# Kernel tuning notes

Hardware: AMD Instinct MI355X
Metric: run time of the kernel (lower is better)

The kernel has to match this reference:

```python
import jax, jax.numpy as jnp
import numpy as np

B, C, T = 16, 192, 4096
K = 5
L = 16


def conv1d(x, w, b, pad):
    # x: [B, Cin, T], w: [Cout, Cin, K] -> [B, Cout, T]
    y = jax.lax.conv_general_dilated(
        x, w, window_strides=(1,), padding=[(pad, pad)],
        dimension_numbers=("NCH", "OIH", "NCH"))
    return y + b[None, :, None]


def setup_inputs() -> dict:
    key = jax.random.key(0)
    ks = jax.random.split(key, 8)
    scale = 0.1
    x = jax.random.normal(ks[0], (B, C, T), dtype=jnp.float32)
    mask = jnp.ones((B, 1, T), dtype=jnp.float32)
    # in_layers: Conv1d(C -> 2C, K), stacked over layers (weight-norm folded)
    W_in = jax.random.normal(ks[1], (L, 2 * C, C, K), dtype=jnp.float32) * scale
    b_in = jax.random.normal(ks[2], (L, 2 * C), dtype=jnp.float32) * scale
    # res_skip layers 0..L-2: Conv1d(C -> 2C, 1)
    W_rs = jax.random.normal(ks[3], (L - 1, 2 * C, C, 1), dtype=jnp.float32) * scale
    b_rs = jax.random.normal(ks[4], (L - 1, 2 * C), dtype=jnp.float32) * scale
    # last res_skip layer: Conv1d(C -> C, 1)
    W_last = jax.random.normal(ks[5], (C, C, 1), dtype=jnp.float32) * scale
    b_last = jax.random.normal(ks[6], (C,), dtype=jnp.float32) * scale
    return {"x": x, "mask": mask, "W_in": W_in, "b_in": b_in,
            "W_rs": W_rs, "b_rs": b_rs, "W_last": W_last, "b_last": b_last}


def reference(x, mask, W_in, b_in, W_rs, b_rs, W_last, b_last):
    pad = K // 2  # dilation_rate == 1, so padding is 'same'
    o = jnp.zeros_like(x)
    for i in range(L):
        x_in = conv1d(x, W_in[i], b_in[i], pad)          # [B, 2C, T]
        x1, x2 = x_in[:, :C], x_in[:, C:]
        acts = jnp.tanh(x1) * jax.nn.sigmoid(x2)          # gated activation (dropout=0)
        if i == L - 1:
            o = o + conv1d(acts, W_last, b_last, 0)
        else:
            rs = conv1d(acts, W_rs[i], b_rs[i], 0)        # [B, 2C, T]
            x = (x + rs[:, :C]) * mask                    # residual
            o = o + rs[:, C:]                              # skip
    return o * mask
```

## Files before the change

kernel.cpp:

```cpp
#include <hip/hip_runtime.h>
#include <hip/hip_bf16.h>

#define C 192
#define T 4096
#define L 16
#define BATCH 16
#define NT 64
#define XR 72
#define CPAD 200

#define CONV_TAP_STRIDE 73728
#define MT_STRIDE       3072
#define ICC_STRIDE      512

typedef __attribute__((ext_vector_type(8))) _Float16 half8;
typedef __attribute__((ext_vector_type(4))) _Float16 half4;
typedef __attribute__((ext_vector_type(4))) float f32x4;

__device__ __forceinline__ float gatefn(float x1, float x2) {
    float ax = fabsf(x1);
    float e  = __expf(-2.f * ax);
    float th = __builtin_copysignf((1.f - e) / (1.f + e), x1);
    float sg = 1.f / (1.f + __expf(-x2));
    return th * sg;
}

__global__ __launch_bounds__(256)
void fmt_win(const float* __restrict__ W, _Float16* __restrict__ dst, int total) {
    int gid = blockIdx.x * 256 + threadIdx.x;
    if (gid >= total) return;
    int lane = gid & 63; int r = gid >> 6;
    int icc = r % 6; r /= 6;
    int mt  = r % 24; r /= 24;
    int tap = r % 5;  int l = r / 5;
    int oc  = mt * 16 + (lane & 15);
    int ic0 = icc * 32 + (lane >> 4) * 8;
    const float* s = W + ((size_t)((l * 384 + oc) * 192 + ic0)) * 5 + tap;
    half8 v;
    #pragma unroll
    for (int i = 0; i < 8; ++i) v[i] = (_Float16)s[(size_t)i * 5];
    *reinterpret_cast<half8*>(dst + (size_t)gid * 8) = v;
}

__global__ __launch_bounds__(256)
void fmt_w11(const float* __restrict__ W, _Float16* __restrict__ dst, int mtc, int total) {
    int gid = blockIdx.x * 256 + threadIdx.x;
    if (gid >= total) return;
    int lane = gid & 63; int r = gid >> 6;
    int icc = r % 6; r /= 6;
    int mt  = r % mtc; int l = r / mtc;
    int oc  = mt * 16 + (lane & 15);
    int ic0 = icc * 32 + (lane >> 4) * 8;
    const float* s = W + (size_t)(l * (mtc * 16) + oc) * 192 + ic0;
    half8 v;
    #pragma unroll
    for (int i = 0; i < 8; ++i) v[i] = (_Float16)s[i];
    *reinterpret_cast<half8*>(dst + (size_t)gid * 8) = v;
}

__global__ __launch_bounds__(256)
void xpose(const float* __restrict__ x, _Float16* __restrict__ xh, _Float16* __restrict__ xl)
{
    __shared__ float tile[C][65];
    const int t0 = blockIdx.x * 64;
    const int b  = blockIdx.y;
    const float* xg = x + (size_t)b * C * T;
    for (int idx = threadIdx.x; idx < C * 16; idx += 256) {
        int ch = idx & 15, c = idx >> 4;
        f32x4 v = *reinterpret_cast<const f32x4*>(xg + (size_t)c * T + t0 + ch * 4);
        #pragma unroll
        for (int q = 0; q < 4; ++q) tile[c][ch * 4 + q] = v[q];
    }
    __syncthreads();
    for (int idx = threadIdx.x; idx < 64 * 24; idx += 256) {
        int cc = idx % 24, t = idx / 24;
        half8 h8, l8;
        #pragma unroll
        for (int i = 0; i < 8; ++i) {
            float v = tile[cc * 8 + i][t];
            _Float16 h = (_Float16)v;
            h8[i] = h;
            l8[i] = (_Float16)(v - (float)h);
        }
        size_t off = (size_t)b * T * C + (size_t)(t0 + t) * C + cc * 8;
        *reinterpret_cast<half8*>(xh + off) = h8;
        *reinterpret_cast<half8*>(xl + off) = l8;
    }
}

template<bool FIRST, bool LAST>
__global__ __launch_bounds__(256, 2)
void wnet_layer(const _Float16* __restrict__ xhin, const _Float16* __restrict__ xlin,
                _Float16* __restrict__ xhout, _Float16* __restrict__ xlout,
                const float* __restrict__ mask,
                const _Float16* __restrict__ wc,
                const float* __restrict__ bc,
                const _Float16* __restrict__ wr,
                const float* __restrict__ br,
                float* __restrict__ o)
{
    __shared__ __align__(16) _Float16 xhi[XR * CPAD];

    const int tid = threadIdx.x;
    const int t0  = blockIdx.x * NT;
    const int b   = blockIdx.y;

    {
        const _Float16* gh = xhin + (size_t)b * T * C;
        for (int idx = tid; idx < XR * 24; idx += 256) {
            int chunk = idx % 24;
            int r     = idx / 24;
            int t = t0 - 4 + r;
            half8 v = {};
            if (t >= 0 && t < T)
                v = *reinterpret_cast<const half8*>(gh + (size_t)t * C + chunk * 8);
            *reinterpret_cast<half8*>(&xhi[r * CPAD + chunk * 8]) = v;
        }
    }
    __syncthreads();

    const int lane = tid & 63;
    const int wm   = tid >> 6;
    const int col  = lane & 15;
    const int sg   = lane >> 4;

    int wbase[6];
    #pragma unroll
    for (int q = 0; q < 6; ++q) {
        int h = q / 3, j = q % 3;
        int mt = h * 12 + wm * 3 + j;
        wbase[q] = mt * MT_STRIDE + lane * 8;
    }

    f32x4 acc[3][2][4];
    #pragma unroll
    for (int j = 0; j < 3; ++j)
    #pragma unroll
    for (int h = 0; h < 2; ++h) {
        f32x4 bv = *reinterpret_cast<const f32x4*>(bc + (h * 12 + wm * 3 + j) * 16 + sg * 4);
        #pragma unroll
        for (int p = 0; p < 4; ++p) acc[j][h][p] = bv;
    }

    half8 hA[6], hB[6];
    #pragma unroll
    for (int q = 0; q < 6; ++q)
        hA[q] = *reinterpret_cast<const half8*>(wc + wbase[q]);

    auto convstep = [&](int icc, half8 (&curH)[6], half8 (&nxtH)[6],
                        size_t tapoff, size_t ntapoff, int tap) {
        const size_t coff = tapoff + (size_t)icc * ICC_STRIDE;
        const size_t noff = (icc == 5) ? ntapoff : coff + ICC_STRIDE;
        #pragma unroll
        for (int q = 0; q < 6; ++q)
            nxtH[q] = *reinterpret_cast<const half8*>(wc + noff + wbase[q]);
        half8 bh[4];
        #pragma unroll
        for (int p = 0; p < 4; ++p) {
            int off = (p * 16 + col + tap + 2) * CPAD + icc * 32 + sg * 8;
            bh[p] = *reinterpret_cast<const half8*>(&xhi[off]);
        }
        __builtin_amdgcn_sched_barrier(0);
        __builtin_amdgcn_s_setprio(1);
        #pragma unroll
        for (int h = 0; h < 2; ++h)
        #pragma unroll
        for (int j = 0; j < 3; ++j)
        #pragma unroll
        for (int p = 0; p < 4; ++p)
            acc[j][h][p] = __builtin_amdgcn_mfma_f32_16x16x32_f16(
                curH[h * 3 + j], bh[p], acc[j][h][p], 0, 0, 0);
        __builtin_amdgcn_s_setprio(0);
    };

    for (int tap = 0; tap < 5; ++tap) {
        const size_t tapoff  = (size_t)tap * CONV_TAP_STRIDE;
        const size_t ntapoff = (size_t)(tap < 4 ? tap + 1 : 4) * CONV_TAP_STRIDE;
        #pragma unroll
        for (int ih = 0; ih < 3; ++ih) {
            convstep(2 * ih,     hA, hB, tapoff, ntapoff, tap);
            convstep(2 * ih + 1, hB, hA, tapoff, ntapoff, tap);
        }
    }

    half4 xresh[3][4];
    if constexpr (!LAST) {
        #pragma unroll
        for (int p = 0; p < 4; ++p) {
            const int row = p * 16 + col + 4;
            #pragma unroll
            for (int j = 0; j < 3; ++j) {
                const int ch = (wm * 3 + j) * 16 + sg * 4;
                xresh[j][p] = *reinterpret_cast<const half4*>(&xhi[row * CPAD + ch]);
            }
        }
    }
    __syncthreads();

    #pragma unroll
    for (int j = 0; j < 3; ++j)
    #pragma unroll
    for (int p = 0; p < 4; ++p) {
        const int tt = p * 16 + col;
        const int ch = (wm * 3 + j) * 16 + sg * 4;
        half4 av;
        #pragma unroll
        for (int i = 0; i < 4; ++i)
            av[i] = (_Float16)gatefn(acc[j][0][p][i], acc[j][1][p][i]);
        *reinterpret_cast<half4*>(&xhi[tt * CPAD + ch]) = av;
    }
    __syncthreads();

    const float* mb = mask + (size_t)b * T;
    float mv[4];
    #pragma unroll
    for (int p = 0; p < 4; ++p) mv[p] = mb[t0 + p * 16 + col];

    constexpr int HN = LAST ? 1 : 2;
    #pragma unroll
    for (int h = 0; h < HN; ++h) {
        f32x4 a2[3][4];
        #pragma unroll
        for (int j = 0; j < 3; ++j) {
            f32x4 bv = *reinterpret_cast<const f32x4*>(br + (h * 12 + wm * 3 + j) * 16 + sg * 4);
            #pragma unroll
            for (int p = 0; p < 4; ++p) a2[j][p] = bv;
        }
        const int* wb = wbase + h * 3;

        half8 rA[3], rB[3];
        #pragma unroll
        for (int q = 0; q < 3; ++q)
            rA[q] = *reinterpret_cast<const half8*>(wr + wb[q]);

        auto r1step = [&](int icc, half8 (&cur)[3], half8 (&nxt)[3]) {
            const size_t noff = (size_t)(icc < 5 ? icc + 1 : 5) * ICC_STRIDE;
            #pragma unroll
            for (int q = 0; q < 3; ++q)
                nxt[q] = *reinterpret_cast<const half8*>(wr + noff + wb[q]);
            half8 bah[4];
            #pragma unroll
            for (int p = 0; p < 4; ++p) {
                int off = (p * 16 + col) * CPAD + icc * 32 + sg * 8;
                bah[p] = *reinterpret_cast<const half8*>(&xhi[off]);
            }
            __builtin_amdgcn_sched_barrier(0);
            __builtin_amdgcn_s_setprio(1);
            #pragma unroll
            for (int j = 0; j < 3; ++j)
            #pragma unroll
            for (int p = 0; p < 4; ++p)
                a2[j][p] = __builtin_amdgcn_mfma_f32_16x16x32_f16(
                    cur[j], bah[p], a2[j][p], 0, 0, 0);
            __builtin_amdgcn_s_setprio(0);
        };

        #pragma unroll
        for (int ih = 0; ih < 3; ++ih) {
            r1step(2 * ih,     rA, rB);
            r1step(2 * ih + 1, rB, rA);
        }

        #pragma unroll
        for (int p = 0; p < 4; ++p) {
            const int tt = p * 16 + col;
            const int t  = t0 + tt;
            #pragma unroll
            for (int j = 0; j < 3; ++j) {
                const int ch = (wm * 3 + j) * 16 + sg * 4;
                if constexpr (LAST) {
                    float* op = o + ((size_t)b * C + ch) * T + t;
                    #pragma unroll
                    for (int i = 0; i < 4; ++i)
                        op[(size_t)i * T] = (op[(size_t)i * T] + a2[j][p][i]) * mv[p];
                } else if (h == 0) {
                    size_t off = (size_t)b * T * C + (size_t)t * C + ch;
                    half4 xl4 = *reinterpret_cast<const half4*>(xlin + off);
                    half4 h4, l4;
                    #pragma unroll
                    for (int i = 0; i < 4; ++i) {
                        float xm = (float)xresh[j][p][i] + (float)xl4[i];
                        float nx = (xm + a2[j][p][i]) * mv[p];
                        _Float16 hh = (_Float16)nx;
                        h4[i] = hh;
                        l4[i] = (_Float16)(nx - (float)hh);
                    }
                    *reinterpret_cast<half4*>(xhout + off) = h4;
                    *reinterpret_cast<half4*>(xlout + off) = l4;
                } else {
                    float* op = o + ((size_t)b * C + ch) * T + t;
                    #pragma unroll
                    for (int i = 0; i < 4; ++i) {
                        if constexpr (FIRST) op[(size_t)i * T] = a2[j][p][i];
                        else                 op[(size_t)i * T] += a2[j][p][i];
                    }
                }
            }
        }
    }
}

#define WIN_STRIDE ((size_t)5 * 24 * 6 * 64 * 8)
#define WRS_STRIDE ((size_t)24 * 6 * 64 * 8)

extern "C" void kernel_launch(void* const* d_in, const int* in_sizes, int n_in,
                              void* d_out, int out_size, void* d_ws, size_t ws_size,
                              hipStream_t stream)
{
    const float* x      = (const float*)d_in[0];
    const float* mask   = (const float*)d_in[1];
    const float* W_in   = (const float*)d_in[2];
    const float* b_in   = (const float*)d_in[3];
    const float* W_rs   = (const float*)d_in[4];
    const float* b_rs   = (const float*)d_in[5];
    const float* W_last = (const float*)d_in[6];
    const float* b_last = (const float*)d_in[7];
    float* o = (float*)d_out;

    const size_t WIN_N = (size_t)L * WIN_STRIDE;
    const size_t WRS_N = (size_t)(L - 1) * WRS_STRIDE;
    const size_t WL_N  = (size_t)12 * 6 * 64 * 8;
    const size_t P     = (size_t)BATCH * T * C;
    _Float16* wc  = (_Float16*)d_ws;
    _Float16* wr  = wc + WIN_N;
    _Float16* wl  = wr + WRS_N;
    _Float16* xah = wl + WL_N;
    _Float16* xal = xah + P;
    _Float16* xbh = xal + P;
    _Float16* xbl = xbh + P;

    {
        int tw = (int)(L * 5 * 24 * 6 * 64);
        fmt_win<<<(tw + 255) / 256, 256, 0, stream>>>(W_in, wc, tw);
        int tr = (int)((L - 1) * 24 * 6 * 64);
        fmt_w11<<<(tr + 255) / 256, 256, 0, stream>>>(W_rs, wr, 24, tr);
        int tl = (int)(12 * 6 * 64);
        fmt_w11<<<(tl + 255) / 256, 256, 0, stream>>>(W_last, wl, 12, tl);
        xpose<<<dim3(T / 64, BATCH), 256, 0, stream>>>(x, xah, xal);
    }

    dim3 grid(T / NT, BATCH);
    dim3 block(256);

    _Float16* curh = xah; _Float16* curl = xal;
    _Float16* nxth = xbh; _Float16* nxtl = xbl;

    wnet_layer<true, false><<<grid, block, 0, stream>>>(
        curh, curl, nxth, nxtl, mask,
        wc, b_in, wr, b_rs, o);
    { _Float16* t1 = curh; curh = nxth; nxth = t1;
      _Float16* t2 = curl; curl = nxtl; nxtl = t2; }

    for (int i = 1; i < L - 1; ++i) {
        wnet_layer<false, false><<<grid, block, 0, stream>>>(
            curh, curl, nxth, nxtl, mask,
            wc + (size_t)i * WIN_STRIDE, b_in + (size_t)i * 2 * C,
            wr + (size_t)i * WRS_STRIDE, b_rs + (size_t)i * 2 * C, o);
        { _Float16* t1 = curh; curh = nxth; nxth = t1;
          _Float16* t2 = curl; curl = nxtl; nxtl = t2; }
    }

    wnet_layer<false, true><<<grid, block, 0, stream>>>(
        curh, curl, nullptr, nullptr, mask,
        wc + (size_t)(L - 1) * WIN_STRIDE, b_in + (size_t)(L - 1) * 2 * C,
        wl, b_last, o);
}
```

Baseline: 1.340 ms.

## Fuse residual and skip halves of 1x1 conv into one MFMA pass

```diff
diff --git a/kernel.cpp b/kernel.cpp
--- a/kernel.cpp
+++ b/kernel.cpp
@@ -100,6 +100,7 @@
                 float* __restrict__ o)
 {
     __shared__ __align__(16) _Float16 xhi[XR * CPAD];
+    __shared__ __align__(16) _Float16 xlo[NT * CPAD];
 
     const int tid = threadIdx.x;
     const int t0  = blockIdx.x * NT;
@@ -116,6 +117,16 @@
                 v = *reinterpret_cast<const half8*>(gh + (size_t)t * C + chunk * 8);
             *reinterpret_cast<half8*>(&xhi[r * CPAD + chunk * 8]) = v;
         }
+        if constexpr (!LAST) {
+            const _Float16* gl = xlin + (size_t)b * T * C;
+            for (int idx = tid; idx < NT * 24; idx += 256) {
+                int chunk = idx % 24;
+                int r     = idx / 24;
+                half8 v = *reinterpret_cast<const half8*>(
+                    gl + (size_t)(t0 + r) * C + chunk * 8);
+                *reinterpret_cast<half8*>(&xlo[r * CPAD + chunk * 8]) = v;
+            }
+        }
     }
     __syncthreads();
 
@@ -217,83 +228,83 @@
     for (int p = 0; p < 4; ++p) mv[p] = mb[t0 + p * 16 + col];
 
     constexpr int HN = LAST ? 1 : 2;
+    constexpr int NQ = HN * 3;
+    f32x4 a2[3][HN][4];
+    #pragma unroll
+    for (int j = 0; j < 3; ++j)
     #pragma unroll
     for (int h = 0; h < HN; ++h) {
-        f32x4 a2[3][4];
+        f32x4 bv = *reinterpret_cast<const f32x4*>(br + (h * 12 + wm * 3 + j) * 16 + sg * 4);
+        #pragma unroll
+        for (int p = 0; p < 4; ++p) a2[j][h][p] = bv;
+    }
+
+    half8 rA[NQ], rB[NQ];
+    #pragma unroll
+    for (int q = 0; q < NQ; ++q)
+        rA[q] = *reinterpret_cast<const half8*>(wr + wbase[q]);
+
+    auto r1step = [&](int icc, half8 (&cur)[NQ], half8 (&nxt)[NQ]) {
+        const size_t noff = (size_t)(icc < 5 ? icc + 1 : 5) * ICC_STRIDE;
+        #pragma unroll
+        for (int q = 0; q < NQ; ++q)
+            nxt[q] = *reinterpret_cast<const half8*>(wr + noff + wbase[q]);
+        half8 bah[4];
+        #pragma unroll
+        for (int p = 0; p < 4; ++p) {
+            int off = (p * 16 + col) * CPAD + icc * 32 + sg * 8;
+            bah[p] = *reinterpret_cast<const half8*>(&xhi[off]);
+        }
+        __builtin_amdgcn_sched_barrier(0);
+        __builtin_amdgcn_s_setprio(1);
+        #pragma unroll
+        for (int h = 0; h < HN; ++h)
+        #pragma unroll
+        for (int j = 0; j < 3; ++j)
+        #pragma unroll
+        for (int p = 0; p < 4; ++p)
+            a2[j][h][p] = __builtin_amdgcn_mfma_f32_16x16x32_f16(
+                cur[h * 3 + j], bah[p], a2[j][h][p], 0, 0, 0);
+        __builtin_amdgcn_s_setprio(0);
+    };
+
+    #pragma unroll
+    for (int ih = 0; ih < 3; ++ih) {
+        r1step(2 * ih,     rA, rB);
+        r1step(2 * ih + 1, rB, rA);
+    }
+
+    #pragma unroll
+    for (int p = 0; p < 4; ++p) {
+        const int tt = p * 16 + col;
+        const int t  = t0 + tt;
         #pragma unroll
         for (int j = 0; j < 3; ++j) {
-            f32x4 bv = *reinterpret_cast<const f32x4*>(br + (h * 12 + wm * 3 + j) * 16 + sg * 4);
-            #pragma unroll
-            for (int p = 0; p < 4; ++p) a2[j][p] = bv;
-        }
-        const int* wb = wbase + h * 3;
-
-        half8 rA[3], rB[3];
-        #pragma unroll
-        for (int q = 0; q < 3; ++q)
-            rA[q] = *reinterpret_cast<const half8*>(wr + wb[q]);
-
-        auto r1step = [&](int icc, half8 (&cur)[3], half8 (&nxt)[3]) {
-            const size_t noff = (size_t)(icc < 5 ? icc + 1 : 5) * ICC_STRIDE;
-            #pragma unroll
-            for (int q = 0; q < 3; ++q)
-                nxt[q] = *reinterpret_cast<const half8*>(wr + noff + wb[q]);
-            half8 bah[4];
-            #pragma unroll
-            for (int p = 0; p < 4; ++p) {
-                int off = (p * 16 + col) * CPAD + icc * 32 + sg * 8;
-                bah[p] = *reinterpret_cast<const half8*>(&xhi[off]);
-            }
-            __builtin_amdgcn_sched_barrier(0);
-            __builtin_amdgcn_s_setprio(1);
-            #pragma unroll
-            for (int j = 0; j < 3; ++j)
-            #pragma unroll
-            for (int p = 0; p < 4; ++p)
-                a2[j][p] = __builtin_amdgcn_mfma_f32_16x16x32_f16(
-                    cur[j], bah[p], a2[j][p], 0, 0, 0);
-            __builtin_amdgcn_s_setprio(0);
-        };
-
-        #pragma unroll
-        for (int ih = 0; ih < 3; ++ih) {
-            r1step(2 * ih,     rA, rB);
-            r1step(2 * ih + 1, rB, rA);
-        }
-
-        #pragma unroll
-        for (int p = 0; p < 4; ++p) {
-            const int tt = p * 16 + col;
-            const int t  = t0 + tt;
-            #pragma unroll
-            for (int j = 0; j < 3; ++j) {
-                const int ch = (wm * 3 + j) * 16 + sg * 4;
-                if constexpr (LAST) {
-                    float* op = o + ((size_t)b * C + ch) * T + t;
-                    #pragma unroll
-                    for (int i = 0; i < 4; ++i)
-                        op[(size_t)i * T] = (op[(size_t)i * T] + a2[j][p][i]) * mv[p];
-                } else if (h == 0) {
-                    size_t off = (size_t)b * T * C + (size_t)t * C + ch;
-                    half4 xl4 = *reinterpret_cast<const half4*>(xlin + off);
-                    half4 h4, l4;
-                    #pragma unroll
-                    for (int i = 0; i < 4; ++i) {
-                        float xm = (float)xresh[j][p][i] + (float)xl4[i];
-                        float nx = (xm + a2[j][p][i]) * mv[p];
-                        _Float16 hh = (_Float16)nx;
-                        h4[i] = hh;
-                        l4[i] = (_Float16)(nx - (float)hh);
-                    }
-                    *reinterpret_cast<half4*>(xhout + off) = h4;
-                    *reinterpret_cast<half4*>(xlout + off) = l4;
-                } else {
-                    float* op = o + ((size_t)b * C + ch) * T + t;
-                    #pragma unroll
-                    for (int i = 0; i < 4; ++i) {
-                        if constexpr (FIRST) op[(size_t)i * T] = a2[j][p][i];
-                        else                 op[(size_t)i * T] += a2[j][p][i];
-                    }
+            const int ch = (wm * 3 + j) * 16 + sg * 4;
+            if constexpr (LAST) {
+                float* op = o + ((size_t)b * C + ch) * T + t;
+                #pragma unroll
+                for (int i = 0; i < 4; ++i)
+                    op[(size_t)i * T] = (op[(size_t)i * T] + a2[j][0][p][i]) * mv[p];
+            } else {
+                size_t off = (size_t)b * T * C + (size_t)t * C + ch;
+                half4 xl4 = *reinterpret_cast<const half4*>(&xlo[tt * CPAD + ch]);
+                half4 h4, l4;
+                #pragma unroll
+                for (int i = 0; i < 4; ++i) {
+                    float xm = (float)xresh[j][p][i] + (float)xl4[i];
+                    float nx = (xm + a2[j][0][p][i]) * mv[p];
+                    _Float16 hh = (_Float16)nx;
+                    h4[i] = hh;
+                    l4[i] = (_Float16)(nx - (float)hh);
+                }
+                *reinterpret_cast<half4*>(xhout + off) = h4;
+                *reinterpret_cast<half4*>(xlout + off) = l4;
+                float* op = o + ((size_t)b * C + ch) * T + t;
+                #pragma unroll
+                for (int i = 0; i < 4; ++i) {
+                    if constexpr (FIRST) op[(size_t)i * T] = a2[j][1][p][i];
+                    else                 op[(size_t)i * T] += a2[j][1][p][i];
                 }
             }
         }
```

Result: no change. 1.337 ms (median of 3 runs) (-0.2%).
